# Optimization experiments

Hardware: AMD Instinct MI355X
Metric: run time of the kernel (lower is better)

Reference implementation:

```python
import jax, jax.numpy as jnp
import numpy as np

N_NODES = 100000
N_EDGES = 1600000
IN_DIM = 128
OUT_DIM = 32
N_HEADS = 4
NEG_SLOPE = 0.2  # DGL GATConv default LeakyReLU negative slope


def setup_inputs() -> dict:
    key = jax.random.key(0)
    k_h, k_src, k_dst, k_w, k_al, k_ar = jax.random.split(key, 6)
    h = jax.random.normal(k_h, (N_NODES, IN_DIM), dtype=jnp.float32)
    src = jax.random.randint(k_src, (N_EDGES,), 0, N_NODES, dtype=jnp.int32)
    dst = jnp.sort(jax.random.randint(k_dst, (N_EDGES,), 0, N_NODES, dtype=jnp.int32))
    # Xavier-ish init scale
    W = jax.random.normal(k_w, (IN_DIM, N_HEADS * OUT_DIM), dtype=jnp.float32) / np.sqrt(IN_DIM)
    attn_l = jax.random.normal(k_al, (N_HEADS, OUT_DIM), dtype=jnp.float32) / np.sqrt(OUT_DIM)
    attn_r = jax.random.normal(k_ar, (N_HEADS, OUT_DIM), dtype=jnp.float32) / np.sqrt(OUT_DIM)
    bias = jnp.zeros((N_HEADS * OUT_DIM,), dtype=jnp.float32)
    return {"h": h, "src": src, "dst": dst, "W": W, "attn_l": attn_l, "attn_r": attn_r, "bias": bias}


def reference(h, src, dst, W, attn_l, attn_r, bias):
    # Eval-mode GATConv (feat_drop / attn_drop disabled).
    N = h.shape[0]
    # Linear projection -> [N, H, D]
    feat = (h @ W).reshape(N, N_HEADS, OUT_DIM)
    # Per-node attention logits: el/er [N, H]
    el = jnp.einsum('nhd,hd->nh', feat, attn_l)
    er = jnp.einsum('nhd,hd->nh', feat, attn_r)
    # Edge scores: e = LeakyReLU(el[src] + er[dst])  -> [E, H]
    e = el[src] + er[dst]
    e = jnp.where(e > 0, e, NEG_SLOPE * e)
    # Segment softmax over incoming edges of each destination node
    e_max = jax.ops.segment_max(e, dst, num_segments=N, indices_are_sorted=True)
    e_exp = jnp.exp(e - e_max[dst])
    denom = jax.ops.segment_sum(e_exp, dst, num_segments=N, indices_are_sorted=True)
    alpha = e_exp / denom[dst]  # [E, H]
    # Weighted aggregate: sum_e alpha[e] * feat[src[e]] per destination
    msg = feat[src] * alpha[:, :, None]  # [E, H, D]
    rst = jax.ops.segment_sum(msg, dst, num_segments=N, indices_are_sorted=True)  # [N, H, D]
    # Bias + ReLU activation (GATLayer default activation=F.relu)
    rst = rst + bias.reshape(1, N_HEADS, OUT_DIM)
    return jax.nn.relu(rst)
```

## Files before the change

### kernel.cpp

```cpp
#include <hip/hip_runtime.h>
#include <hip/hip_fp16.h>
#include <math.h>

#define NEG_SLOPE 0.2f

typedef _Float16 f16x2 __attribute__((ext_vector_type(2)));
typedef _Float16 f16x8 __attribute__((ext_vector_type(8)));
typedef float f32x4 __attribute__((ext_vector_type(4)));

__device__ __forceinline__ float fdot2f(unsigned int a, unsigned int b, float c) {
#if __has_builtin(__builtin_amdgcn_fdot2)
    return __builtin_amdgcn_fdot2(__builtin_bit_cast(f16x2, a),
                                  __builtin_bit_cast(f16x2, b), c, false);
#else
    __half2 ah = __builtin_bit_cast(__half2, a), bh = __builtin_bit_cast(__half2, b);
    float2 af = __half22float2(ah), bf = __half22float2(bh);
    return c + af.x * bf.x + af.y * bf.y;
#endif
}

__global__ __launch_bounds__(256) void prep_seg_kernel(
    const float* __restrict__ W, __half* __restrict__ w16t,
    const int* __restrict__ dst, int* __restrict__ off, int E, int N)
{
    const int b = blockIdx.x;
    if (b < 64) {
        int tid = b * 256 + threadIdx.x;
        int c = tid >> 7, k = tid & 127;
        w16t[c * 128 + k] = __float2half(W[k * 128 + c]);
        return;
    }
    int i = (b - 64) * 256 + threadIdx.x;
    if (i >= E) return;
    int d = dst[i];
    int prev = (i == 0) ? -1 : dst[i - 1];
    for (int n = prev + 1; n <= d; ++n) off[n] = i;
    if (i == E - 1) {
        for (int n = d + 1; n <= N; ++n) off[n] = E;
    }
}

__global__ __launch_bounds__(256) void proj_kernel(
    const float* __restrict__ h, const __half* __restrict__ w16t,
    const float* __restrict__ attn_l, const float* __restrict__ attn_r,
    __half* __restrict__ feat, float* __restrict__ el, float* __restrict__ er,
    int N)
{
    __shared__ __half hl[64 * 128];
    __shared__ __half wl[128 * 128];
    const int t = threadIdx.x;
    const int nodeBase = blockIdx.x * 64;

#pragma unroll
    for (int i = 0; i < 8; ++i) {
        int ch = t + i * 256;
        int col = ch >> 4, k8 = ch & 15;
        uint4 v = *(const uint4*)(w16t + col * 128 + k8 * 8);
        int byte = col * 256 + k8 * 16;
        *(uint4*)((char*)wl + (byte ^ ((col & 7) << 4))) = v;
    }
#pragma unroll
    for (int i = 0; i < 8; ++i) {
        int slot = t + i * 256;
        int row = slot >> 5, c4 = slot & 31;
        int gn = nodeBase + row;
        float4 v = make_float4(0.f, 0.f, 0.f, 0.f);
        if (gn < N) v = *(const float4*)(h + (size_t)gn * 128 + c4 * 4);
        __half2 p0 = __floats2half2_rn(v.x, v.y);
        __half2 p1 = __floats2half2_rn(v.z, v.w);
        uint2 u = make_uint2(__builtin_bit_cast(unsigned int, p0),
                             __builtin_bit_cast(unsigned int, p1));
        int byte = row * 256 + c4 * 8;
        *(uint2*)((char*)hl + (byte ^ ((row & 7) << 4))) = u;
    }
    __syncthreads();

    const int l = t & 63, wave = t >> 6;
    const int arow = wave * 16 + (l & 15);
    const int kg = l >> 4;
    f32x4 acc[8];
#pragma unroll
    for (int i = 0; i < 8; ++i) acc[i] = (f32x4){0.f, 0.f, 0.f, 0.f};

#pragma unroll
    for (int kt = 0; kt < 4; ++kt) {
        const int kb = (kt * 32 + kg * 8) * 2;
        f16x8 a = *(const f16x8*)((const char*)hl +
                    ((arow * 256 + kb) ^ ((arow & 7) << 4)));
#pragma unroll
        for (int ct = 0; ct < 8; ++ct) {
            int bcol = ct * 16 + (l & 15);
            f16x8 b = *(const f16x8*)((const char*)wl +
                        ((bcol * 256 + kb) ^ ((bcol & 7) << 4)));
            acc[ct] = __builtin_amdgcn_mfma_f32_16x16x32_f16(a, b, acc[ct], 0, 0, 0);
        }
    }

    __syncthreads();
    const int colLo = l & 15;
    const int rowHi = wave * 16 + (l >> 4) * 4;
#pragma unroll
    for (int ct = 0; ct < 8; ++ct) {
#pragma unroll
        for (int r = 0; r < 4; ++r) {
            int row = rowHi + r;
            int byte = row * 256 + (ct * 16 + colLo) * 2;
            *(__half*)((char*)hl + (byte ^ ((row & 7) << 4))) = __float2half(acc[ct][r]);
        }
    }

    float pl[4][4], pr[4][4];
#pragma unroll
    for (int hh = 0; hh < 4; ++hh) {
        float al0 = attn_l[hh * 32 + colLo];
        float al1 = attn_l[hh * 32 + 16 + colLo];
        float ar0 = attn_r[hh * 32 + colLo];
        float ar1 = attn_r[hh * 32 + 16 + colLo];
#pragma unroll
        for (int r = 0; r < 4; ++r) {
            pl[hh][r] = acc[2 * hh][r] * al0 + acc[2 * hh + 1][r] * al1;
            pr[hh][r] = acc[2 * hh][r] * ar0 + acc[2 * hh + 1][r] * ar1;
        }
    }
#pragma unroll
    for (int msk = 1; msk <= 8; msk <<= 1) {
#pragma unroll
        for (int hh = 0; hh < 4; ++hh)
#pragma unroll
            for (int r = 0; r < 4; ++r) {
                pl[hh][r] += __shfl_xor(pl[hh][r], msk);
                pr[hh][r] += __shfl_xor(pr[hh][r], msk);
            }
    }
    if (colLo == 0) {
#pragma unroll
        for (int r = 0; r < 4; ++r) {
            int node = nodeBase + rowHi + r;
            if (node < N) {
                *(float4*)(el + (size_t)node * 4) =
                    make_float4(pl[0][r], pl[1][r], pl[2][r], pl[3][r]);
                *(float4*)(er + (size_t)node * 4) =
                    make_float4(pr[0][r], pr[1][r], pr[2][r], pr[3][r]);
            }
        }
    }
    __syncthreads();

    char* featB = (char*)feat + (size_t)nodeBase * 256;
#pragma unroll
    for (int i = 0; i < 4; ++i) {
        int c = t + i * 256;
        int row = c >> 4;
        uint4 v = *(const uint4*)((const char*)hl + ((c * 16) ^ ((row & 7) << 4)));
        if (nodeBase + row < N) *(uint4*)(featB + c * 16) = v;
    }
}

__global__ __launch_bounds__(256) void edgew_kernel(
    const float* __restrict__ el, const float* __restrict__ er,
    const int* __restrict__ src, const int* __restrict__ dst,
    __half* __restrict__ w_t, int E)
{
    int e = blockIdx.x * 256 + threadIdx.x;
    if (e >= E) return;
    int sv = src[e], dv = dst[e];
    float4 a = *(const float4*)(el + (size_t)sv * 4);
    float4 b = *(const float4*)(er + (size_t)dv * 4);
    float s0 = a.x + b.x, s1 = a.y + b.y, s2 = a.z + b.z, s3 = a.w + b.w;
    s0 = s0 > 0.f ? s0 : NEG_SLOPE * s0;
    s1 = s1 > 0.f ? s1 : NEG_SLOPE * s1;
    s2 = s2 > 0.f ? s2 : NEG_SLOPE * s2;
    s3 = s3 > 0.f ? s3 : NEG_SLOPE * s3;
    w_t[e]                 = __float2half(__expf(s0));
    w_t[(size_t)E + e]     = __float2half(__expf(s1));
    w_t[(size_t)2 * E + e] = __float2half(__expf(s2));
    w_t[(size_t)3 * E + e] = __float2half(__expf(s3));
}

__global__ __launch_bounds__(256) void aggregate_kernel(
    const __half* __restrict__ feat, const __half* __restrict__ w_t,
    const int* __restrict__ off, const int* __restrict__ src,
    const float* __restrict__ bias, float* __restrict__ out, int N, int E)
{
    const int wid = (int)((blockIdx.x * blockDim.x + threadIdx.x) >> 6);
    const int l = threadIdx.x & 63;
    if (wid >= N) return;
    const int n = __builtin_amdgcn_readfirstlane(wid);
    int s = off[n];
    const int e = off[n + 1];
    const int f0 = 2 * l;
    const float b0 = bias[f0], b1 = bias[f0 + 1];
    float* outp = out + (size_t)n * 128;
    if (s >= e) {
        outp[f0] = fmaxf(b0, 0.f);
        outp[f0 + 1] = fmaxf(b1, 0.f);
        return;
    }

    const __half* wp = w_t + (size_t)(l >> 4) * E;
    float ax = 0.f, ay = 0.f, dn = 0.f;
    const unsigned int one2 = 0x3C003C00u;

    if (s & 1) {
        int sv = src[s];
        float w = __half2float(wp[s]);
        __half2 gh = *(const __half2*)(feat + (size_t)sv * 128 + f0);
        float2 fv = __half22float2(gh);
        ax += w * fv.x; ay += w * fv.y; dn += w;
        ++s;
    }

    int ei = s;
    for (; ei + 16 <= e; ei += 16) {
        int sv[16];
#pragma unroll
        for (int k = 0; k < 16; ++k) sv[k] = src[ei + k];
        unsigned int w2[8];
#pragma unroll
        for (int k = 0; k < 8; ++k) w2[k] = *(const unsigned int*)(wp + ei + 2 * k);
        unsigned int g[16];
#pragma unroll
        for (int k = 0; k < 16; ++k)
            g[k] = *(const unsigned int*)(feat + (size_t)sv[k] * 128 + f0);
#pragma unroll
        for (int k = 0; k < 8; ++k) {
            unsigned int lo = __builtin_amdgcn_perm(g[2 * k + 1], g[2 * k], 0x05040100u);
            unsigned int hi = __builtin_amdgcn_perm(g[2 * k + 1], g[2 * k], 0x07060302u);
            ax = fdot2f(w2[k], lo, ax);
            ay = fdot2f(w2[k], hi, ay);
            dn = fdot2f(w2[k], one2, dn);
        }
    }
    if (ei + 8 <= e) {
        int sv[8];
#pragma unroll
        for (int k = 0; k < 8; ++k) sv[k] = src[ei + k];
        unsigned int w2[4];
#pragma unroll
        for (int k = 0; k < 4; ++k) w2[k] = *(const unsigned int*)(wp + ei + 2 * k);
        unsigned int g[8];
#pragma unroll
        for (int k = 0; k < 8; ++k)
            g[k] = *(const unsigned int*)(feat + (size_t)sv[k] * 128 + f0);
#pragma unroll
        for (int k = 0; k < 4; ++k) {
            unsigned int lo = __builtin_amdgcn_perm(g[2 * k + 1], g[2 * k], 0x05040100u);
            unsigned int hi = __builtin_amdgcn_perm(g[2 * k + 1], g[2 * k], 0x07060302u);
            ax = fdot2f(w2[k], lo, ax);
            ay = fdot2f(w2[k], hi, ay);
            dn = fdot2f(w2[k], one2, dn);
        }
        ei += 8;
    }
    if (ei + 4 <= e) {
        int sv0 = src[ei], sv1 = src[ei + 1], sv2 = src[ei + 2], sv3 = src[ei + 3];
        unsigned int w2a = *(const unsigned int*)(wp + ei);
        unsigned int w2b = *(const unsigned int*)(wp + ei + 2);
        unsigned int g0 = *(const unsigned int*)(feat + (size_t)sv0 * 128 + f0);
        unsigned int g1 = *(const unsigned int*)(feat + (size_t)sv1 * 128 + f0);
        unsigned int g2 = *(const unsigned int*)(feat + (size_t)sv2 * 128 + f0);
        unsigned int g3 = *(const unsigned int*)(feat + (size_t)sv3 * 128 + f0);
        unsigned int lo = __builtin_amdgcn_perm(g1, g0, 0x05040100u);
        unsigned int hi = __builtin_amdgcn_perm(g1, g0, 0x07060302u);
        ax = fdot2f(w2a, lo, ax); ay = fdot2f(w2a, hi, ay); dn = fdot2f(w2a, one2, dn);
        lo = __builtin_amdgcn_perm(g3, g2, 0x05040100u);
        hi = __builtin_amdgcn_perm(g3, g2, 0x07060302u);
        ax = fdot2f(w2b, lo, ax); ay = fdot2f(w2b, hi, ay); dn = fdot2f(w2b, one2, dn);
        ei += 4;
    }
    if (ei + 2 <= e) {
        int sv0 = src[ei], sv1 = src[ei + 1];
        unsigned int w2 = *(const unsigned int*)(wp + ei);
        unsigned int g0 = *(const unsigned int*)(feat + (size_t)sv0 * 128 + f0);
        unsigned int g1 = *(const unsigned int*)(feat + (size_t)sv1 * 128 + f0);
        unsigned int lo = __builtin_amdgcn_perm(g1, g0, 0x05040100u);
        unsigned int hi = __builtin_amdgcn_perm(g1, g0, 0x07060302u);
        ax = fdot2f(w2, lo, ax); ay = fdot2f(w2, hi, ay); dn = fdot2f(w2, one2, dn);
        ei += 2;
    }
    if (ei < e) {
        int sv = src[ei];
        float w = __half2float(wp[ei]);
        __half2 gh = *(const __half2*)(feat + (size_t)sv * 128 + f0);
        float2 fv = __half22float2(gh);
        ax += w * fv.x; ay += w * fv.y; dn += w;
    }
    const float inv = 1.f / dn;
    *(float2*)(outp + f0) = make_float2(fmaxf(ax * inv + b0, 0.f),
                                        fmaxf(ay * inv + b1, 0.f));
}

extern "C" void kernel_launch(void* const* d_in, const int* in_sizes, int n_in,
                              void* d_out, int out_size, void* d_ws, size_t ws_size,
                              hipStream_t stream)
{
    const float* h      = (const float*)d_in[0];
    const int*   src    = (const int*)d_in[1];
    const int*   dst    = (const int*)d_in[2];
    const float* W      = (const float*)d_in[3];
    const float* attn_l = (const float*)d_in[4];
    const float* attn_r = (const float*)d_in[5];
    const float* bias   = (const float*)d_in[6];
    const int N = in_sizes[0] / 128;
    const int E = in_sizes[1];
    float* out = (float*)d_out;

    char* ws = (char*)d_ws;
    __half* feat = (__half*)ws;            ws += (size_t)N * 128 * sizeof(__half);
    float*  el   = (float*)ws;             ws += (size_t)N * 4 * sizeof(float);
    float*  er   = (float*)ws;             ws += (size_t)N * 4 * sizeof(float);
    __half* w_t  = (__half*)ws;            ws += (size_t)E * 4 * sizeof(__half);
    __half* w16t = (__half*)ws;            ws += 128 * 128 * sizeof(__half);
    int*    off  = (int*)ws;

    hipLaunchKernelGGL(prep_seg_kernel, dim3(64 + (E + 255) / 256), dim3(256), 0, stream,
                       W, w16t, dst, off, E, N);
    hipLaunchKernelGGL(proj_kernel, dim3((N + 63) / 64), dim3(256), 0, stream,
                       h, w16t, attn_l, attn_r, feat, el, er, N);
    hipLaunchKernelGGL(edgew_kernel, dim3((E + 255) / 256), dim3(256), 0, stream,
                       el, er, src, dst, w_t, E);
    hipLaunchKernelGGL(aggregate_kernel, dim3((N + 3) / 4), dim3(256), 0, stream,
                       feat, w_t, off, src, bias, out, N, E);
}
```

Before: 110.1 us.

## Fuse edge-weight computation into aggregation kernel, drop edge weight buffer

Removes the separate edge-weight kernel and its E x 4 fp16 intermediate buffer, and instead computes LeakyReLU and exp of el[src]+er[dst] inside the aggregation loop. Each lane gathers el for its head per source node alongside the feature gather. This saves one launch and the write and re-read of the weight array. In exchange it adds per-lane scalar gathers of el and duplicates exp work across the 16 lanes that share a head.

```diff
diff --git a/kernel.cpp b/kernel.cpp
--- a/kernel.cpp
+++ b/kernel.cpp
@@ -16,6 +16,14 @@
     __half2 ah = __builtin_bit_cast(__half2, a), bh = __builtin_bit_cast(__half2, b);
     float2 af = __half22float2(ah), bf = __half22float2(bh);
     return c + af.x * bf.x + af.y * bf.y;
+#endif
+}
+
+__device__ __forceinline__ unsigned int packw(float a, float b) {
+#if __has_builtin(__builtin_amdgcn_cvt_pkrtz)
+    return __builtin_bit_cast(unsigned int, __builtin_amdgcn_cvt_pkrtz(a, b));
+#else
+    return __builtin_bit_cast(unsigned int, __floats2half2_rn(a, b));
 #endif
 }
 
@@ -156,39 +164,20 @@
     }
 }
 
-__global__ __launch_bounds__(256) void edgew_kernel(
-    const float* __restrict__ el, const float* __restrict__ er,
-    const int* __restrict__ src, const int* __restrict__ dst,
-    __half* __restrict__ w_t, int E)
-{
-    int e = blockIdx.x * 256 + threadIdx.x;
-    if (e >= E) return;
-    int sv = src[e], dv = dst[e];
-    float4 a = *(const float4*)(el + (size_t)sv * 4);
-    float4 b = *(const float4*)(er + (size_t)dv * 4);
-    float s0 = a.x + b.x, s1 = a.y + b.y, s2 = a.z + b.z, s3 = a.w + b.w;
-    s0 = s0 > 0.f ? s0 : NEG_SLOPE * s0;
-    s1 = s1 > 0.f ? s1 : NEG_SLOPE * s1;
-    s2 = s2 > 0.f ? s2 : NEG_SLOPE * s2;
-    s3 = s3 > 0.f ? s3 : NEG_SLOPE * s3;
-    w_t[e]                 = __float2half(__expf(s0));
-    w_t[(size_t)E + e]     = __float2half(__expf(s1));
-    w_t[(size_t)2 * E + e] = __float2half(__expf(s2));
-    w_t[(size_t)3 * E + e] = __float2half(__expf(s3));
-}
-
 __global__ __launch_bounds__(256) void aggregate_kernel(
-    const __half* __restrict__ feat, const __half* __restrict__ w_t,
-    const int* __restrict__ off, const int* __restrict__ src,
-    const float* __restrict__ bias, float* __restrict__ out, int N, int E)
+    const __half* __restrict__ feat, const float* __restrict__ el,
+    const float* __restrict__ er, const int* __restrict__ off,
+    const int* __restrict__ src, const float* __restrict__ bias,
+    float* __restrict__ out, int N)
 {
     const int wid = (int)((blockIdx.x * blockDim.x + threadIdx.x) >> 6);
     const int l = threadIdx.x & 63;
     if (wid >= N) return;
     const int n = __builtin_amdgcn_readfirstlane(wid);
-    int s = off[n];
+    const int s = off[n];
     const int e = off[n + 1];
     const int f0 = 2 * l;
+    const int hm = l >> 4;
     const float b0 = bias[f0], b1 = bias[f0 + 1];
     float* outp = out + (size_t)n * 128;
     if (s >= e) {
@@ -197,69 +186,83 @@
         return;
     }
 
-    const __half* wp = w_t + (size_t)(l >> 4) * E;
+    const float er_mine = er[n * 4 + hm];
     float ax = 0.f, ay = 0.f, dn = 0.f;
     const unsigned int one2 = 0x3C003C00u;
-
-    if (s & 1) {
-        int sv = src[s];
-        float w = __half2float(wp[s]);
-        __half2 gh = *(const __half2*)(feat + (size_t)sv * 128 + f0);
-        float2 fv = __half22float2(gh);
-        ax += w * fv.x; ay += w * fv.y; dn += w;
-        ++s;
-    }
 
     int ei = s;
     for (; ei + 16 <= e; ei += 16) {
         int sv[16];
 #pragma unroll
         for (int k = 0; k < 16; ++k) sv[k] = src[ei + k];
-        unsigned int w2[8];
-#pragma unroll
-        for (int k = 0; k < 8; ++k) w2[k] = *(const unsigned int*)(wp + ei + 2 * k);
+        float elv[16];
+#pragma unroll
+        for (int k = 0; k < 16; ++k) elv[k] = el[(size_t)sv[k] * 4 + hm];
         unsigned int g[16];
 #pragma unroll
         for (int k = 0; k < 16; ++k)
             g[k] = *(const unsigned int*)(feat + (size_t)sv[k] * 128 + f0);
+        float w[16];
+#pragma unroll
+        for (int k = 0; k < 16; ++k) {
+            float sc = elv[k] + er_mine;
+            sc = sc > 0.f ? sc : NEG_SLOPE * sc;
+            w[k] = __expf(sc);
+        }
 #pragma unroll
         for (int k = 0; k < 8; ++k) {
+            unsigned int w2 = packw(w[2 * k], w[2 * k + 1]);
             unsigned int lo = __builtin_amdgcn_perm(g[2 * k + 1], g[2 * k], 0x05040100u);
             unsigned int hi = __builtin_amdgcn_perm(g[2 * k + 1], g[2 * k], 0x07060302u);
-            ax = fdot2f(w2[k], lo, ax);
-            ay = fdot2f(w2[k], hi, ay);
-            dn = fdot2f(w2[k], one2, dn);
+            ax = fdot2f(w2, lo, ax);
+            ay = fdot2f(w2, hi, ay);
+            dn = fdot2f(w2, one2, dn);
         }
     }
     if (ei + 8 <= e) {
         int sv[8];
 #pragma unroll
         for (int k = 0; k < 8; ++k) sv[k] = src[ei + k];
-        unsigned int w2[4];
-#pragma unroll
-        for (int k = 0; k < 4; ++k) w2[k] = *(const unsigned int*)(wp + ei + 2 * k);
+        float elv[8];
+#pragma unroll
+        for (int k = 0; k < 8; ++k) elv[k] = el[(size_t)sv[k] * 4 + hm];
         unsigned int g[8];
 #pragma unroll
         for (int k = 0; k < 8; ++k)
             g[k] = *(const unsigned int*)(feat + (size_t)sv[k] * 128 + f0);
+        float w[8];
+#pragma unroll
+        for (int k = 0; k < 8; ++k) {
+            float sc = elv[k] + er_mine;
+            sc = sc > 0.f ? sc : NEG_SLOPE * sc;
+            w[k] = __expf(sc);
+        }
 #pragma unroll
         for (int k = 0; k < 4; ++k) {
+            unsigned int w2 = packw(w[2 * k], w[2 * k + 1]);
             unsigned int lo = __builtin_amdgcn_perm(g[2 * k + 1], g[2 * k], 0x05040100u);
             unsigned int hi = __builtin_amdgcn_perm(g[2 * k + 1], g[2 * k], 0x07060302u);
-            ax = fdot2f(w2[k], lo, ax);
-            ay = fdot2f(w2[k], hi, ay);
-            dn = fdot2f(w2[k], one2, dn);
+            ax = fdot2f(w2, lo, ax);
+            ay = fdot2f(w2, hi, ay);
+            dn = fdot2f(w2, one2, dn);
         }
         ei += 8;
     }
     if (ei + 4 <= e) {
         int sv0 = src[ei], sv1 = src[ei + 1], sv2 = src[ei + 2], sv3 = src[ei + 3];
-        unsigned int w2a = *(const unsigned int*)(wp + ei);
-        unsigned int w2b = *(const unsigned int*)(wp + ei + 2);
+        float e0 = el[(size_t)sv0 * 4 + hm], e1 = el[(size_t)sv1 * 4 + hm];
+        float e2 = el[(size_t)sv2 * 4 + hm], e3 = el[(size_t)sv3 * 4 + hm];
         unsigned int g0 = *(const unsigned int*)(feat + (size_t)sv0 * 128 + f0);
         unsigned int g1 = *(const unsigned int*)(feat + (size_t)sv1 * 128 + f0);
         unsigned int g2 = *(const unsigned int*)(feat + (size_t)sv2 * 128 + f0);
         unsigned int g3 = *(const unsigned int*)(feat + (size_t)sv3 * 128 + f0);
+        float s0 = e0 + er_mine, s1 = e1 + er_mine, s2 = e2 + er_mine, s3 = e3 + er_mine;
+        s0 = s0 > 0.f ? s0 : NEG_SLOPE * s0;
+        s1 = s1 > 0.f ? s1 : NEG_SLOPE * s1;
+        s2 = s2 > 0.f ? s2 : NEG_SLOPE * s2;
+        s3 = s3 > 0.f ? s3 : NEG_SLOPE * s3;
+        unsigned int w2a = packw(__expf(s0), __expf(s1));
+        unsigned int w2b = packw(__expf(s2), __expf(s3));
         unsigned int lo = __builtin_amdgcn_perm(g1, g0, 0x05040100u);
         unsigned int hi = __builtin_amdgcn_perm(g1, g0, 0x07060302u);
         ax = fdot2f(w2a, lo, ax); ay = fdot2f(w2a, hi, ay); dn = fdot2f(w2a, one2, dn);
@@ -268,19 +271,11 @@
         ax = fdot2f(w2b, lo, ax); ay = fdot2f(w2b, hi, ay); dn = fdot2f(w2b, one2, dn);
         ei += 4;
     }
-    if (ei + 2 <= e) {
-        int sv0 = src[ei], sv1 = src[ei + 1];
-        unsigned int w2 = *(const unsigned int*)(wp + ei);
-        unsigned int g0 = *(const unsigned int*)(feat + (size_t)sv0 * 128 + f0);
-        unsigned int g1 = *(const unsigned int*)(feat + (size_t)sv1 * 128 + f0);
-        unsigned int lo = __builtin_amdgcn_perm(g1, g0, 0x05040100u);
-        unsigned int hi = __builtin_amdgcn_perm(g1, g0, 0x07060302u);
-        ax = fdot2f(w2, lo, ax); ay = fdot2f(w2, hi, ay); dn = fdot2f(w2, one2, dn);
-        ei += 2;
-    }
-    if (ei < e) {
+    for (; ei < e; ++ei) {
         int sv = src[ei];
-        float w = __half2float(wp[ei]);
+        float sc = el[(size_t)sv * 4 + hm] + er_mine;
+        sc = sc > 0.f ? sc : NEG_SLOPE * sc;
+        float w = __expf(sc);
         __half2 gh = *(const __half2*)(feat + (size_t)sv * 128 + f0);
         float2 fv = __half22float2(gh);
         ax += w * fv.x; ay += w * fv.y; dn += w;
@@ -309,7 +304,6 @@
     __half* feat = (__half*)ws;            ws += (size_t)N * 128 * sizeof(__half);
     float*  el   = (float*)ws;             ws += (size_t)N * 4 * sizeof(float);
     float*  er   = (float*)ws;             ws += (size_t)N * 4 * sizeof(float);
-    __half* w_t  = (__half*)ws;            ws += (size_t)E * 4 * sizeof(__half);
     __half* w16t = (__half*)ws;            ws += 128 * 128 * sizeof(__half);
     int*    off  = (int*)ws;
 
@@ -317,8 +311,6 @@
                        W, w16t, dst, off, E, N);
     hipLaunchKernelGGL(proj_kernel, dim3((N + 63) / 64), dim3(256), 0, stream,
                        h, w16t, attn_l, attn_r, feat, el, er, N);
-    hipLaunchKernelGGL(edgew_kernel, dim3((E + 255) / 256), dim3(256), 0, stream,
-                       el, er, src, dst, w_t, E);
     hipLaunchKernelGGL(aggregate_kernel, dim3((N + 3) / 4), dim3(256), 0, stream,
-                       feat, w_t, off, src, bias, out, N, E);
-}
+                       feat, el, er, off, src, bias, out, N);
+}
```

After: 108.9 us. About the same (-1.1%).

## Split each node's edge list across two waves and combine partials in LDS

Applied to the files above, without the earlier changes.

The aggregate kernel now gives each destination node two wavefronts. Each wave processes half of the node's edge pairs, and the second wave's partial sums are reduced through shared memory before the output is written. The goal is more memory-level parallelism for the gather-bound aggregation, since average degree is about 16 and a single wave has few gathers in flight. The cost is a block-wide barrier, LDS traffic, and shorter per-wave loops that may fall through to the smaller unrolled tails more often.

```diff
diff --git a/kernel.cpp b/kernel.cpp
--- a/kernel.cpp
+++ b/kernel.cpp
@@ -182,112 +182,143 @@
     const int* __restrict__ off, const int* __restrict__ src,
     const float* __restrict__ bias, float* __restrict__ out, int N, int E)
 {
-    const int wid = (int)((blockIdx.x * blockDim.x + threadIdx.x) >> 6);
-    const int l = threadIdx.x & 63;
-    if (wid >= N) return;
-    const int n = __builtin_amdgcn_readfirstlane(wid);
+    __shared__ float part_ax[2][64];
+    __shared__ float part_ay[2][64];
+    __shared__ float part_dn[2][64];
+
+    const int wave = threadIdx.x >> 6, l = threadIdx.x & 63;
+    const int p = wave >> 1, sub = wave & 1;
+    const int n0 = blockIdx.x * 2 + p;
+    const bool active = (n0 < N);
+    const int n = __builtin_amdgcn_readfirstlane(active ? n0 : 0);
     int s = off[n];
     const int e = off[n + 1];
     const int f0 = 2 * l;
-    const float b0 = bias[f0], b1 = bias[f0 + 1];
-    float* outp = out + (size_t)n * 128;
-    if (s >= e) {
-        outp[f0] = fmaxf(b0, 0.f);
-        outp[f0 + 1] = fmaxf(b1, 0.f);
-        return;
-    }
-
-    const __half* wp = w_t + (size_t)(l >> 4) * E;
+    const int hm = l >> 4;
+    const __half* wp = w_t + (size_t)hm * E;
     float ax = 0.f, ay = 0.f, dn = 0.f;
     const unsigned int one2 = 0x3C003C00u;
 
-    if (s & 1) {
-        int sv = src[s];
-        float w = __half2float(wp[s]);
-        __half2 gh = *(const __half2*)(feat + (size_t)sv * 128 + f0);
-        float2 fv = __half22float2(gh);
-        ax += w * fv.x; ay += w * fv.y; dn += w;
-        ++s;
-    }
-
-    int ei = s;
-    for (; ei + 16 <= e; ei += 16) {
-        int sv[16];
-#pragma unroll
-        for (int k = 0; k < 16; ++k) sv[k] = src[ei + k];
-        unsigned int w2[8];
-#pragma unroll
-        for (int k = 0; k < 8; ++k) w2[k] = *(const unsigned int*)(wp + ei + 2 * k);
-        unsigned int g[16];
-#pragma unroll
-        for (int k = 0; k < 16; ++k)
-            g[k] = *(const unsigned int*)(feat + (size_t)sv[k] * 128 + f0);
-#pragma unroll
-        for (int k = 0; k < 8; ++k) {
-            unsigned int lo = __builtin_amdgcn_perm(g[2 * k + 1], g[2 * k], 0x05040100u);
-            unsigned int hi = __builtin_amdgcn_perm(g[2 * k + 1], g[2 * k], 0x07060302u);
-            ax = fdot2f(w2[k], lo, ax);
-            ay = fdot2f(w2[k], hi, ay);
-            dn = fdot2f(w2[k], one2, dn);
-        }
-    }
-    if (ei + 8 <= e) {
-        int sv[8];
-#pragma unroll
-        for (int k = 0; k < 8; ++k) sv[k] = src[ei + k];
-        unsigned int w2[4];
-#pragma unroll
-        for (int k = 0; k < 4; ++k) w2[k] = *(const unsigned int*)(wp + ei + 2 * k);
-        unsigned int g[8];
-#pragma unroll
-        for (int k = 0; k < 8; ++k)
-            g[k] = *(const unsigned int*)(feat + (size_t)sv[k] * 128 + f0);
-#pragma unroll
-        for (int k = 0; k < 4; ++k) {
-            unsigned int lo = __builtin_amdgcn_perm(g[2 * k + 1], g[2 * k], 0x05040100u);
-            unsigned int hi = __builtin_amdgcn_perm(g[2 * k + 1], g[2 * k], 0x07060302u);
-            ax = fdot2f(w2[k], lo, ax);
-            ay = fdot2f(w2[k], hi, ay);
-            dn = fdot2f(w2[k], one2, dn);
-        }
-        ei += 8;
-    }
-    if (ei + 4 <= e) {
-        int sv0 = src[ei], sv1 = src[ei + 1], sv2 = src[ei + 2], sv3 = src[ei + 3];
-        unsigned int w2a = *(const unsigned int*)(wp + ei);
-        unsigned int w2b = *(const unsigned int*)(wp + ei + 2);
-        unsigned int g0 = *(const unsigned int*)(feat + (size_t)sv0 * 128 + f0);
-        unsigned int g1 = *(const unsigned int*)(feat + (size_t)sv1 * 128 + f0);
-        unsigned int g2 = *(const unsigned int*)(feat + (size_t)sv2 * 128 + f0);
-        unsigned int g3 = *(const unsigned int*)(feat + (size_t)sv3 * 128 + f0);
-        unsigned int lo = __builtin_amdgcn_perm(g1, g0, 0x05040100u);
-        unsigned int hi = __builtin_amdgcn_perm(g1, g0, 0x07060302u);
-        ax = fdot2f(w2a, lo, ax); ay = fdot2f(w2a, hi, ay); dn = fdot2f(w2a, one2, dn);
-        lo = __builtin_amdgcn_perm(g3, g2, 0x05040100u);
-        hi = __builtin_amdgcn_perm(g3, g2, 0x07060302u);
-        ax = fdot2f(w2b, lo, ax); ay = fdot2f(w2b, hi, ay); dn = fdot2f(w2b, one2, dn);
-        ei += 4;
-    }
-    if (ei + 2 <= e) {
-        int sv0 = src[ei], sv1 = src[ei + 1];
-        unsigned int w2 = *(const unsigned int*)(wp + ei);
-        unsigned int g0 = *(const unsigned int*)(feat + (size_t)sv0 * 128 + f0);
-        unsigned int g1 = *(const unsigned int*)(feat + (size_t)sv1 * 128 + f0);
-        unsigned int lo = __builtin_amdgcn_perm(g1, g0, 0x05040100u);
-        unsigned int hi = __builtin_amdgcn_perm(g1, g0, 0x07060302u);
-        ax = fdot2f(w2, lo, ax); ay = fdot2f(w2, hi, ay); dn = fdot2f(w2, one2, dn);
-        ei += 2;
-    }
-    if (ei < e) {
-        int sv = src[ei];
-        float w = __half2float(wp[ei]);
-        __half2 gh = *(const __half2*)(feat + (size_t)sv * 128 + f0);
-        float2 fv = __half22float2(gh);
-        ax += w * fv.x; ay += w * fv.y; dn += w;
-    }
-    const float inv = 1.f / dn;
-    *(float2*)(outp + f0) = make_float2(fmaxf(ax * inv + b0, 0.f),
-                                        fmaxf(ay * inv + b1, 0.f));
+    if (active && s < e) {
+        int a0 = s;
+        if (s & 1) {
+            if (sub == 0) {
+                int sv = src[s];
+                float w = __half2float(wp[s]);
+                __half2 gh = *(const __half2*)(feat + (size_t)sv * 128 + f0);
+                float2 fv = __half22float2(gh);
+                ax += w * fv.x; ay += w * fv.y; dn += w;
+            }
+            a0 = s + 1;
+        }
+        const int cnt = e - a0;
+        const int pairs = cnt >> 1;
+        const int ph0 = pairs >> 1;
+        int lo, hi;
+        if (sub == 0) { lo = a0;           hi = a0 + 2 * ph0;   }
+        else          { lo = a0 + 2 * ph0; hi = a0 + 2 * pairs; }
+
+        int ei = lo;
+        for (; ei + 16 <= hi; ei += 16) {
+            int sv[16];
+#pragma unroll
+            for (int k = 0; k < 16; ++k) sv[k] = src[ei + k];
+            const __half* wpb = wp + ei;
+            unsigned int w2[8];
+#pragma unroll
+            for (int k = 0; k < 8; ++k) w2[k] = *(const unsigned int*)(wpb + 2 * k);
+            unsigned int g[16];
+#pragma unroll
+            for (int k = 0; k < 16; ++k)
+                g[k] = *(const unsigned int*)(feat + (size_t)sv[k] * 128 + f0);
+#pragma unroll
+            for (int k = 0; k < 8; ++k) {
+                unsigned int lo_ = __builtin_amdgcn_perm(g[2 * k + 1], g[2 * k], 0x05040100u);
+                unsigned int hi_ = __builtin_amdgcn_perm(g[2 * k + 1], g[2 * k], 0x07060302u);
+                ax = fdot2f(w2[k], lo_, ax);
+                ay = fdot2f(w2[k], hi_, ay);
+                dn = fdot2f(w2[k], one2, dn);
+            }
+        }
+        if (ei + 8 <= hi) {
+            int sv[8];
+#pragma unroll
+            for (int k = 0; k < 8; ++k) sv[k] = src[ei + k];
+            const __half* wpb = wp + ei;
+            unsigned int w2[4];
+#pragma unroll
+            for (int k = 0; k < 4; ++k) w2[k] = *(const unsigned int*)(wpb + 2 * k);
+            unsigned int g[8];
+#pragma unroll
+            for (int k = 0; k < 8; ++k)
+                g[k] = *(const unsigned int*)(feat + (size_t)sv[k] * 128 + f0);
+#pragma unroll
+            for (int k = 0; k < 4; ++k) {
+                unsigned int lo_ = __builtin_amdgcn_perm(g[2 * k + 1], g[2 * k], 0x05040100u);
+                unsigned int hi_ = __builtin_amdgcn_perm(g[2 * k + 1], g[2 * k], 0x07060302u);
+                ax = fdot2f(w2[k], lo_, ax);
+                ay = fdot2f(w2[k], hi_, ay);
+                dn = fdot2f(w2[k], one2, dn);
+            }
+            ei += 8;
+        }
+        if (ei + 4 <= hi) {
+            int sv0 = src[ei], sv1 = src[ei + 1], sv2 = src[ei + 2], sv3 = src[ei + 3];
+            unsigned int w2a = *(const unsigned int*)(wp + ei);
+            unsigned int w2b = *(const unsigned int*)(wp + ei + 2);
+            unsigned int g0 = *(const unsigned int*)(feat + (size_t)sv0 * 128 + f0);
+            unsigned int g1 = *(const unsigned int*)(feat + (size_t)sv1 * 128 + f0);
+            unsigned int g2 = *(const unsigned int*)(feat + (size_t)sv2 * 128 + f0);
+            unsigned int g3 = *(const unsigned int*)(feat + (size_t)sv3 * 128 + f0);
+            unsigned int lo_ = __builtin_amdgcn_perm(g1, g0, 0x05040100u);
+            unsigned int hi_ = __builtin_amdgcn_perm(g1, g0, 0x07060302u);
+            ax = fdot2f(w2a, lo_, ax); ay = fdot2f(w2a, hi_, ay); dn = fdot2f(w2a, one2, dn);
+            lo_ = __builtin_amdgcn_perm(g3, g2, 0x05040100u);
+            hi_ = __builtin_amdgcn_perm(g3, g2, 0x07060302u);
+            ax = fdot2f(w2b, lo_, ax); ay = fdot2f(w2b, hi_, ay); dn = fdot2f(w2b, one2, dn);
+            ei += 4;
+        }
+        if (ei + 2 <= hi) {
+            int sv0 = src[ei], sv1 = src[ei + 1];
+            unsigned int w2 = *(const unsigned int*)(wp + ei);
+            unsigned int g0 = *(const unsigned int*)(feat + (size_t)sv0 * 128 + f0);
+            unsigned int g1 = *(const unsigned int*)(feat + (size_t)sv1 * 128 + f0);
+            unsigned int lo_ = __builtin_amdgcn_perm(g1, g0, 0x05040100u);
+            unsigned int hi_ = __builtin_amdgcn_perm(g1, g0, 0x07060302u);
+            ax = fdot2f(w2, lo_, ax); ay = fdot2f(w2, hi_, ay); dn = fdot2f(w2, one2, dn);
+            ei += 2;
+        }
+        if (sub == 1 && (cnt & 1)) {
+            int idx = e - 1;
+            int sv = src[idx];
+            float w = __half2float(wp[idx]);
+            __half2 gh = *(const __half2*)(feat + (size_t)sv * 128 + f0);
+            float2 fv = __half22float2(gh);
+            ax += w * fv.x; ay += w * fv.y; dn += w;
+        }
+    }
+
+    if (sub == 1) {
+        part_ax[p][l] = ax;
+        part_ay[p][l] = ay;
+        part_dn[p][l] = dn;
+    }
+    __syncthreads();
+    if (active && sub == 0) {
+        const float b0 = bias[f0], b1 = bias[f0 + 1];
+        float* outp = out + (size_t)n * 128;
+        if (s >= e) {
+            outp[f0]     = fmaxf(b0, 0.f);
+            outp[f0 + 1] = fmaxf(b1, 0.f);
+        } else {
+            ax += part_ax[p][l];
+            ay += part_ay[p][l];
+            dn += part_dn[p][l];
+            const float inv = 1.f / dn;
+            *(float2*)(outp + f0) = make_float2(fmaxf(ax * inv + b0, 0.f),
+                                                fmaxf(ay * inv + b1, 0.f));
+        }
+    }
 }
 
 extern "C" void kernel_launch(void* const* d_in, const int* in_sizes, int n_in,
@@ -319,6 +350,6 @@
                        h, w16t, attn_l, attn_r, feat, el, er, N);
     hipLaunchKernelGGL(edgew_kernel, dim3((E + 255) / 256), dim3(256), 0, stream,
                        el, er, src, dst, w_t, E);
-    hipLaunchKernelGGL(aggregate_kernel, dim3((N + 3) / 4), dim3(256), 0, stream,
+    hipLaunchKernelGGL(aggregate_kernel, dim3((N + 1) / 2), dim3(256), 0, stream,
                        feat, w_t, off, src, bias, out, N, E);
 }
```

Result: slower. 132.5 us (+20.3%).
